# Optimization experiments

Hardware: AMD Instinct MI355X
Metric: run time of the kernel (lower is better)

## Reference

```python
import jax, jax.numpy as jnp
import numpy as np

NORM_EPS = 1e-12  # torch F.normalize default eps (module's self.eps is unused)


def setup_inputs() -> dict:
    key = jax.random.key(0)
    k1, k2 = jax.random.split(key)
    src_feat = jax.random.normal(k1, (4, 2048, 128), dtype=jnp.float32)
    tgt_feat = jax.random.normal(k2, (4, 2048, 128), dtype=jnp.float32)
    return {"src_feat": src_feat, "tgt_feat": tgt_feat}


def reference(src_feat, tgt_feat):
    # src_feat: [B,N,C], tgt_feat: [B,M,C]
    # Cosine similarity via normalized matmul instead of [B,N,M,C] broadcast.
    src_sq = jnp.sum(src_feat * src_feat, axis=-1)          # [B,N]
    tgt_sq = jnp.sum(tgt_feat * tgt_feat, axis=-1)          # [B,M]
    src_n = src_feat / jnp.maximum(jnp.sqrt(src_sq), NORM_EPS)[..., None]
    tgt_n = tgt_feat / jnp.maximum(jnp.sqrt(tgt_sq), NORM_EPS)[..., None]
    cosine_sim = jnp.einsum('bnc,bmc->bnm', src_n, tgt_n)   # [B,N,M]
    # Squared L2 distance via ||s||^2 + ||t||^2 - 2 s.t (clamped for numerics)
    dots = jnp.einsum('bnc,bmc->bnm', src_feat, tgt_feat)   # [B,N,M]
    dist_sq = src_sq[:, :, None] + tgt_sq[:, None, :] - 2.0 * dots
    feat_dist = jnp.sqrt(jnp.maximum(dist_sq, 0.0))
    feat_dist_normalized = 1.0 / (1.0 + feat_dist)
    # [B,N,M,2]
    return jnp.stack([cosine_sim, feat_dist_normalized], axis=-1)
```

## Files before the change

### kernel.cpp

```cpp
#include <hip/hip_runtime.h>

#define BATCH 4
#define NDIM 2048
#define MDIM 2048
#define CDIM 128
#define NROWS (BATCH * NDIM)

typedef short bf16x8 __attribute__((ext_vector_type(8)));
typedef float f32x4  __attribute__((ext_vector_type(4)));

__device__ __forceinline__ unsigned short f2bf(float f) {
    union { float f; unsigned int u; } v; v.f = f;
    unsigned int u = v.u;
    return (unsigned short)((u + 0x7FFFu + ((u >> 16) & 1u)) >> 16);
}

__device__ __forceinline__ void gload_lds16(const void* g, void* l) {
    __builtin_amdgcn_global_load_lds(
        (const __attribute__((address_space(1))) void*)g,
        (__attribute__((address_space(3))) void*)l, 16, 0, 0);
}

__global__ __launch_bounds__(256) void prep_kernel(
    const float* __restrict__ src, const float* __restrict__ tgt,
    unsigned short* __restrict__ bf, float* __restrict__ nrm)
{
    int gid = blockIdx.x * 256 + threadIdx.x;
    int row = gid >> 5;
    int l32 = gid & 31;
    const float* base = (row < NROWS)
        ? (src + (size_t)row * CDIM)
        : (tgt + (size_t)(row - NROWS) * CDIM);
    float4 v = ((const float4*)base)[l32];
    float s = v.x * v.x + v.y * v.y + v.z * v.z + v.w * v.w;
    #pragma unroll
    for (int off = 16; off >= 1; off >>= 1) s += __shfl_xor(s, off, 64);
    if (l32 == 0) nrm[row] = s;

    int chunk = l32 >> 1;
    int half  = l32 & 1;
    unsigned short* dst = bf + (size_t)row * CDIM
                        + (((chunk ^ (row & 15)) << 3) + (half << 2));
    ushort4 u;
    u.x = f2bf(v.x); u.y = f2bf(v.y); u.z = f2bf(v.z); u.w = f2bf(v.w);
    *(ushort4*)dst = u;
}

__global__ __launch_bounds__(256, 3) void sim_mfma(
    const unsigned short* __restrict__ bfS, const unsigned short* __restrict__ bfT,
    const float* __restrict__ nrm, float* __restrict__ out)
{
    __shared__ unsigned short As[128 * 128];
    __shared__ unsigned short Bs[64 * 128];

    const int tid = threadIdx.x;
    const int b   = blockIdx.z;
    const int i0  = blockIdx.y << 7;
    const int j0  = blockIdx.x << 6;

    const char* gA = (const char*)(bfS + ((size_t)b * NDIM + i0) * CDIM);
    const char* gB = (const char*)(bfT + ((size_t)b * MDIM + j0) * CDIM);
    char* lA = (char*)As;
    char* lB = (char*)Bs;
    const int t16 = tid << 4;

    #pragma unroll
    for (int it = 0; it < 8; ++it)
        gload_lds16(gA + t16 + it * 4096, lA + t16 + it * 4096);
    #pragma unroll
    for (int it = 0; it < 4; ++it)
        gload_lds16(gB + t16 + it * 4096, lB + t16 + it * 4096);
    __syncthreads();

    const int wave = tid >> 6;
    const int lane = tid & 63;
    const int wm   = (wave & 1) << 6;
    const int wn   = (wave >> 1) << 5;
    const int l16  = lane & 15;
    const int q    = lane >> 4;

    const float* nrmS = nrm + (size_t)b * NDIM + i0;
    const float* nrmT = nrm + (size_t)NROWS + (size_t)b * MDIM + j0;

    float sq[4][4], isq[4][4];
    #pragma unroll
    for (int i = 0; i < 4; ++i) {
        float4 s4v = *(const float4*)&nrmS[wm + (i << 4) + (q << 2)];
        sq[i][0] = s4v.x; sq[i][1] = s4v.y; sq[i][2] = s4v.z; sq[i][3] = s4v.w;
        #pragma unroll
        for (int r = 0; r < 4; ++r)
            isq[i][r] = __builtin_amdgcn_rsqf(fmaxf(sq[i][r], 1e-24f));
    }
    float tq[2], itq[2];
    #pragma unroll
    for (int jh = 0; jh < 2; ++jh) {
        tq[jh]  = nrmT[wn + (jh << 4) + l16];
        itq[jh] = __builtin_amdgcn_rsqf(fmaxf(tq[jh], 1e-24f));
    }

    float2* out2 = (float2*)out;

    #pragma unroll
    for (int jh = 0; jh < 2; ++jh) {
        f32x4 acc[4];
        #pragma unroll
        for (int i = 0; i < 4; ++i) acc[i] = (f32x4){0.f, 0.f, 0.f, 0.f};

        const int brow = wn + (jh << 4) + l16;
        #pragma unroll
        for (int k0 = 0; k0 < 4; ++k0) {
            int chunk = (k0 << 2) + q;
            int swz   = (chunk ^ l16) << 3;
            bf16x8 bv = *(const bf16x8*)&Bs[brow * 128 + swz];
            #pragma unroll
            for (int i = 0; i < 4; ++i) {
                bf16x8 a = *(const bf16x8*)&As[(wm + (i << 4) + l16) * 128 + swz];
                acc[i] = __builtin_amdgcn_mfma_f32_16x16x32_bf16(a, bv, acc[i], 0, 0, 0);
            }
        }

        const int   ncol = wn + (jh << 4) + l16;
        const float tqj  = tq[jh], itj = itq[jh];
        #pragma unroll
        for (int i = 0; i < 4; ++i) {
            #pragma unroll
            for (int r = 0; r < 4; ++r) {
                int mrow = wm + (i << 4) + (q << 2) + r;
                size_t rowbase =
                    ((size_t)b * NDIM + (size_t)(i0 + mrow)) * MDIM + j0;
                float d   = acc[i][r];
                float cs  = d * isq[i][r] * itj;
                float dsq = fmaf(-2.0f, d, sq[i][r] + tqj);
                float fd  = __builtin_amdgcn_sqrtf(fmaxf(dsq, 0.0f));
                float fdn = __builtin_amdgcn_rcpf(1.0f + fd);
                out2[rowbase + ncol] = make_float2(cs, fdn);
            }
        }
    }
}

extern "C" void kernel_launch(void* const* d_in, const int* in_sizes, int n_in,
                              void* d_out, int out_size, void* d_ws, size_t ws_size,
                              hipStream_t stream) {
    const float* src = (const float*)d_in[0];
    const float* tgt = (const float*)d_in[1];
    float* out = (float*)d_out;

    unsigned short* bfS = (unsigned short*)d_ws;
    unsigned short* bfT = bfS + (size_t)NROWS * CDIM;
    float*          nrm = (float*)(bfT + (size_t)NROWS * CDIM);

    prep_kernel<<<dim3(2048), dim3(256), 0, stream>>>(src, tgt, bfS, nrm);

    dim3 grid(MDIM / 64, NDIM / 128, BATCH);
    sim_mfma<<<grid, dim3(256), 0, stream>>>(bfS, bfT, nrm, out);
}
```

Baseline: 144.3 us.

## Shrink tile to 64x64, swizzle block order, use nontemporal output stores

```diff
diff --git a/kernel.cpp b/kernel.cpp
--- a/kernel.cpp
+++ b/kernel.cpp
@@ -8,6 +8,7 @@
 
 typedef short bf16x8 __attribute__((ext_vector_type(8)));
 typedef float f32x4  __attribute__((ext_vector_type(4)));
+typedef float f32x2  __attribute__((ext_vector_type(2)));
 
 __device__ __forceinline__ unsigned short f2bf(float f) {
     union { float f; unsigned int u; } v; v.f = f;
@@ -46,17 +47,19 @@
     *(ushort4*)dst = u;
 }
 
-__global__ __launch_bounds__(256, 3) void sim_mfma(
+__global__ __launch_bounds__(256, 5) void sim_mfma(
     const unsigned short* __restrict__ bfS, const unsigned short* __restrict__ bfT,
     const float* __restrict__ nrm, float* __restrict__ out)
 {
-    __shared__ unsigned short As[128 * 128];
+    __shared__ unsigned short As[64 * 128];
     __shared__ unsigned short Bs[64 * 128];
 
-    const int tid = threadIdx.x;
-    const int b   = blockIdx.z;
-    const int i0  = blockIdx.y << 7;
-    const int j0  = blockIdx.x << 6;
+    const int tid  = threadIdx.x;
+    const int flat = blockIdx.x;
+    const int swb  = (flat & 7) * 512 + (flat >> 3);
+    const int b    = swb >> 10;
+    const int i0   = ((swb >> 5) & 31) << 6;
+    const int j0   = (swb & 31) << 6;
 
     const char* gA = (const char*)(bfS + ((size_t)b * NDIM + i0) * CDIM);
     const char* gB = (const char*)(bfT + ((size_t)b * MDIM + j0) * CDIM);
@@ -65,7 +68,7 @@
     const int t16 = tid << 4;
 
     #pragma unroll
-    for (int it = 0; it < 8; ++it)
+    for (int it = 0; it < 4; ++it)
         gload_lds16(gA + t16 + it * 4096, lA + t16 + it * 4096);
     #pragma unroll
     for (int it = 0; it < 4; ++it)
@@ -74,17 +77,42 @@
 
     const int wave = tid >> 6;
     const int lane = tid & 63;
-    const int wm   = (wave & 1) << 6;
+    const int wm   = (wave & 1) << 5;
     const int wn   = (wave >> 1) << 5;
     const int l16  = lane & 15;
     const int q    = lane >> 4;
 
+    f32x4 acc[2][2];
+    #pragma unroll
+    for (int i = 0; i < 2; ++i)
+        #pragma unroll
+        for (int j = 0; j < 2; ++j) acc[i][j] = (f32x4){0.f, 0.f, 0.f, 0.f};
+
+    #pragma unroll
+    for (int k0 = 0; k0 < 4; ++k0) {
+        int chunk = (k0 << 2) + q;
+        int swz   = (chunk ^ l16) << 3;
+        bf16x8 a[2], bv[2];
+        #pragma unroll
+        for (int i = 0; i < 2; ++i)
+            a[i] = *(const bf16x8*)&As[(wm + (i << 4) + l16) * 128 + swz];
+        #pragma unroll
+        for (int j = 0; j < 2; ++j)
+            bv[j] = *(const bf16x8*)&Bs[(wn + (j << 4) + l16) * 128 + swz];
+        #pragma unroll
+        for (int i = 0; i < 2; ++i)
+            #pragma unroll
+            for (int j = 0; j < 2; ++j)
+                acc[i][j] = __builtin_amdgcn_mfma_f32_16x16x32_bf16(
+                    a[i], bv[j], acc[i][j], 0, 0, 0);
+    }
+
     const float* nrmS = nrm + (size_t)b * NDIM + i0;
     const float* nrmT = nrm + (size_t)NROWS + (size_t)b * MDIM + j0;
 
-    float sq[4][4], isq[4][4];
+    float sq[2][4], isq[2][4];
     #pragma unroll
-    for (int i = 0; i < 4; ++i) {
+    for (int i = 0; i < 2; ++i) {
         float4 s4v = *(const float4*)&nrmS[wm + (i << 4) + (q << 2)];
         sq[i][0] = s4v.x; sq[i][1] = s4v.y; sq[i][2] = s4v.z; sq[i][3] = s4v.w;
         #pragma unroll
@@ -93,47 +121,29 @@
     }
     float tq[2], itq[2];
     #pragma unroll
-    for (int jh = 0; jh < 2; ++jh) {
-        tq[jh]  = nrmT[wn + (jh << 4) + l16];
-        itq[jh] = __builtin_amdgcn_rsqf(fmaxf(tq[jh], 1e-24f));
+    for (int j = 0; j < 2; ++j) {
+        tq[j]  = nrmT[wn + (j << 4) + l16];
+        itq[j] = __builtin_amdgcn_rsqf(fmaxf(tq[j], 1e-24f));
     }
 
-    float2* out2 = (float2*)out;
-
+    f32x2* out2 = (f32x2*)out;
     #pragma unroll
-    for (int jh = 0; jh < 2; ++jh) {
-        f32x4 acc[4];
+    for (int i = 0; i < 2; ++i) {
         #pragma unroll
-        for (int i = 0; i < 4; ++i) acc[i] = (f32x4){0.f, 0.f, 0.f, 0.f};
-
-        const int brow = wn + (jh << 4) + l16;
-        #pragma unroll
-        for (int k0 = 0; k0 < 4; ++k0) {
-            int chunk = (k0 << 2) + q;
-            int swz   = (chunk ^ l16) << 3;
-            bf16x8 bv = *(const bf16x8*)&Bs[brow * 128 + swz];
+        for (int r = 0; r < 4; ++r) {
+            int mrow = wm + (i << 4) + (q << 2) + r;
+            size_t rowbase = ((size_t)b * NDIM + (size_t)(i0 + mrow)) * MDIM + j0;
+            float sqr = sq[i][r], isr = isq[i][r];
             #pragma unroll
-            for (int i = 0; i < 4; ++i) {
-                bf16x8 a = *(const bf16x8*)&As[(wm + (i << 4) + l16) * 128 + swz];
-                acc[i] = __builtin_amdgcn_mfma_f32_16x16x32_bf16(a, bv, acc[i], 0, 0, 0);
-            }
-        }
-
-        const int   ncol = wn + (jh << 4) + l16;
-        const float tqj  = tq[jh], itj = itq[jh];
-        #pragma unroll
-        for (int i = 0; i < 4; ++i) {
-            #pragma unroll
-            for (int r = 0; r < 4; ++r) {
-                int mrow = wm + (i << 4) + (q << 2) + r;
-                size_t rowbase =
-                    ((size_t)b * NDIM + (size_t)(i0 + mrow)) * MDIM + j0;
-                float d   = acc[i][r];
-                float cs  = d * isq[i][r] * itj;
-                float dsq = fmaf(-2.0f, d, sq[i][r] + tqj);
+            for (int j = 0; j < 2; ++j) {
+                int ncol = wn + (j << 4) + l16;
+                float d   = acc[i][j][r];
+                float cs  = d * isr * itq[j];
+                float dsq = fmaf(-2.0f, d, sqr + tq[j]);
                 float fd  = __builtin_amdgcn_sqrtf(fmaxf(dsq, 0.0f));
                 float fdn = __builtin_amdgcn_rcpf(1.0f + fd);
-                out2[rowbase + ncol] = make_float2(cs, fdn);
+                f32x2 o; o.x = cs; o.y = fdn;
+                __builtin_nontemporal_store(o, &out2[rowbase + ncol]);
             }
         }
     }
@@ -152,6 +162,5 @@
 
     prep_kernel<<<dim3(2048), dim3(256), 0, stream>>>(src, tgt, bfS, nrm);
 
-    dim3 grid(MDIM / 64, NDIM / 128, BATCH);
-    sim_mfma<<<grid, dim3(256), 0, stream>>>(bfS, bfT, nrm, out);
+    sim_mfma<<<dim3(4096), dim3(256), 0, stream>>>(bfS, bfT, nrm, out);
 }
```

Result: slower. 148.8 us (+3.1%).
